# Kernel optimization log

Hardware: AMD Instinct MI355X
Metric: run time of the kernel (lower is better)

## Reference

```python
import jax, jax.numpy as jnp
import numpy as np

N, F, H, C = 50000, 128, 4, 32   # nodes, in_channels, heads, hidden_channels
E, R, DE = 800000, 8, 64         # edges, num_relations, edge_dim


def setup_inputs() -> dict:
    key = jax.random.key(0)
    ks = jax.random.split(key, 10)
    x = jax.random.normal(ks[0], (N, F), dtype=jnp.float32)
    edge_index = jax.random.randint(ks[1], (2, E), 0, N, dtype=jnp.int64)
    edge_type = jax.random.randint(ks[2], (E,), 0, R, dtype=jnp.int64)
    s_in = 1.0 / np.sqrt(F)
    s_e = 1.0 / np.sqrt(DE)
    edge_emb = jax.random.normal(ks[3], (R, DE), dtype=jnp.float32)
    Wq = jax.random.normal(ks[4], (F, H * C), dtype=jnp.float32) * s_in
    Wk = jax.random.normal(ks[5], (F, H * C), dtype=jnp.float32) * s_in
    Wv = jax.random.normal(ks[6], (F, H * C), dtype=jnp.float32) * s_in
    We = jax.random.normal(ks[7], (DE, H * C), dtype=jnp.float32) * s_e
    Wskip = jax.random.normal(ks[8], (F, H * C), dtype=jnp.float32) * s_in
    return {"x": x, "edge_index": edge_index, "edge_type": edge_type,
            "edge_emb": edge_emb, "Wq": Wq, "Wk": Wk, "Wv": Wv,
            "We": We, "Wskip": Wskip}


def reference(x, edge_index, edge_type, edge_emb, Wq, Wk, Wv, We, Wskip):
    # TransformerConv (PyG) with edge embeddings, concat heads, root skip, no bias.
    src, dst = edge_index[0], edge_index[1]
    q = (x @ Wq).reshape(N, H, C)
    k = (x @ Wk).reshape(N, H, C)
    v = (x @ Wv).reshape(N, H, C)
    e = (edge_emb[edge_type] @ We).reshape(E, H, C)      # per-edge relation emb
    kj = k[src] + e                                       # [E,H,C]
    logits = (q[dst] * kj).sum(-1) / jnp.sqrt(jnp.float32(C))  # [E,H]
    # segment softmax over incoming edges of each target node
    m = jax.ops.segment_max(logits, dst, num_segments=N)  # [N,H]
    m = jnp.where(jnp.isfinite(m), m, jnp.float32(0.0))
    ex = jnp.exp(logits - m[dst])
    denom = jax.ops.segment_sum(ex, dst, num_segments=N)  # [N,H]
    alpha = ex / (denom[dst] + 1e-16)                     # [E,H]
    msg = (v[src] + e) * alpha[:, :, None]                # [E,H,C]
    out = jax.ops.segment_sum(msg, dst, num_segments=N).reshape(N, H * C)
    return out + x @ Wskip
```

## Files before the change

kernel.cpp:

```cpp
#include <hip/hip_runtime.h>
#include <hip/hip_bf16.h>

#define NN 50000
#define FF 128
#define NH 4
#define CH 32
#define HC 128
#define NE 800000
#define NR 8
#define DEDIM 64
#define NBLK 196
#define HBLK 3125
#define QBLK 250
#define MTILES 3125

typedef __hip_bfloat16 bf16;
typedef __attribute__((ext_vector_type(8))) short short8;
typedef __attribute__((ext_vector_type(4))) float f32x4;

__device__ __forceinline__ float bflo(unsigned u) { return __uint_as_float(u << 16); }
__device__ __forceinline__ float bfhi(unsigned u) { return __uint_as_float(u & 0xFFFF0000u); }

__device__ __forceinline__ unsigned short f2bf(float f) {
  unsigned u = __float_as_uint(f);
  unsigned r = (u + 0x7FFFu + ((u >> 16) & 1u)) >> 16;
  return (unsigned short)r;
}
__device__ __forceinline__ unsigned pack2bf(float lo, float hi) {
  return (unsigned)f2bf(lo) | ((unsigned)f2bf(hi) << 16);
}

template <int ISBF>
__device__ __forceinline__ float ldf(const void* p, size_t i) {
  if (ISBF) return __bfloat162float(((const bf16*)p)[i]);
  return ((const float*)p)[i];
}

__device__ __forceinline__ int idx_at(const void* p, long long i, int is64) {
  if (is64) { long long v = ((const long long*)p)[i]; return (int)v; }
  return ((const int*)p)[i];
}

__global__ __launch_bounds__(256) void k_prep(const unsigned* __restrict__ xw,
    const int* __restrict__ eidx32, const void* __restrict__ etype,
    const void* __restrict__ emb, const void* __restrict__ We,
    int* __restrict__ flag, int* __restrict__ hist, float* __restrict__ ee,
    unsigned* __restrict__ drk, int* __restrict__ setp) {
  __shared__ float es[NR * DEDIM];
  __shared__ int nzIdx, badBf;
  if (blockIdx.x < HBLK) {
    unsigned long long b = __ballot(eidx32[2 * (threadIdx.x & 63) + 1] != 0);
    int is64 = (b == 0ULL);
    int e = blockIdx.x * 256 + threadIdx.x;
    int src = idx_at(eidx32, e, is64);
    int dst = idx_at(eidx32, (long long)NE + e, is64);
    int et  = idx_at(etype, e, is64);
    src = min(max(src, 0), NN - 1);
    dst = min(max(dst, 0), NN - 1);
    et  = min(max(et, 0), NR - 1);
    int rank = atomicAdd(&hist[dst], 1);
    drk[e]  = ((unsigned)dst << 16) | ((unsigned)rank & 0xFFFFu);
    setp[e] = (src << 3) | et;
    return;
  }
  if (threadIdx.x == 0) { nzIdx = 0; badBf = 0; }
  __syncthreads();
  if (threadIdx.x < 128) {
    if (eidx32[2 * threadIdx.x + 1] != 0) atomicAdd(&nzIdx, 1);
    unsigned e = (xw[threadIdx.x] >> 7) & 0xFFu;
    if (e < 90u || e > 140u) atomicAdd(&badBf, 1);
  }
  __syncthreads();
  const int isbf = (badBf == 0);
  if (threadIdx.x == 0) { flag[0] = (nzIdx == 0); flag[1] = isbf; }
  for (int i = threadIdx.x; i < NR * DEDIM; i += 256)
    es[i] = isbf ? ldf<1>(emb, i) : ldf<0>(emb, i);
  __syncthreads();
  for (int o = threadIdx.x; o < NR * HC; o += 256) {
    int r = o >> 7, j = o & 127;
    float acc = 0.f;
    if (isbf) { for (int d = 0; d < DEDIM; ++d) acc += es[r * DEDIM + d] * ldf<1>(We, d * HC + j); }
    else      { for (int d = 0; d < DEDIM; ++d) acc += es[r * DEDIM + d] * ldf<0>(We, d * HC + j); }
    ee[o] = acc;
  }
}

template <int ISBF>
__device__ __forceinline__ void stage_nat(const void* __restrict__ W,
                                          unsigned short* __restrict__ w) {
  if (ISBF) {
    const uint4* s = (const uint4*)W;
    uint4* d = (uint4*)w;
    for (int i = threadIdx.x; i < FF * HC / 8; i += 256) d[i] = s[i];
  } else {
    const float4* s = (const float4*)W;
    short8* d = (short8*)w;
    for (int i = threadIdx.x; i < FF * HC / 8; i += 256) {
      float4 a = s[2 * i], b = s[2 * i + 1];
      short8 o;
      o[0] = (short)f2bf(a.x); o[1] = (short)f2bf(a.y);
      o[2] = (short)f2bf(a.z); o[3] = (short)f2bf(a.w);
      o[4] = (short)f2bf(b.x); o[5] = (short)f2bf(b.y);
      o[6] = (short)f2bf(b.z); o[7] = (short)f2bf(b.w);
      d[i] = o;
    }
  }
}

__device__ __forceinline__ void hoist_nat(const unsigned short* __restrict__ w,
                                          int wv, int quad, int lr,
                                          short8 bf[2][4]) {
#pragma unroll
  for (int t = 0; t < 2; ++t) {
    int ncol = wv * 32 + t * 16 + lr;
#pragma unroll
    for (int kb = 0; kb < 4; ++kb) {
      short8 v;
#pragma unroll
      for (int j = 0; j < 8; ++j)
        v[j] = (short)w[(kb * 32 + quad * 8 + j) * HC + ncol];
      bf[t][kb] = v;
    }
  }
}

template <int ISBF>
__device__ __forceinline__ void qkvs4_body(const void* __restrict__ x,
    const void* __restrict__ Wq, const void* __restrict__ Ws,
    const void* __restrict__ Wk, const void* __restrict__ Wv,
    unsigned short* __restrict__ qb, unsigned* __restrict__ kvb,
    void* __restrict__ out, unsigned short* __restrict__ wt4,
    unsigned char* __restrict__ est) {
  const int tid  = threadIdx.x;
  const int lane = tid & 63;
  const int wv   = tid >> 6;
  const int quad = lane >> 4;
  const int lr   = lane & 15;
  stage_nat<ISBF>(Wq, wt4 + 0 * FF * HC);
  stage_nat<ISBF>(Ws, wt4 + 1 * FF * HC);
  stage_nat<ISBF>(Wk, wt4 + 2 * FF * HC);
  stage_nat<ISBF>(Wv, wt4 + 3 * FF * HC);
  __syncthreads();
  short8 bf[4][2][4];
#pragma unroll
  for (int m = 0; m < 4; ++m)
    hoist_nat(wt4 + m * FF * HC, wv, quad, lr, bf[m]);
  unsigned short* qs  = (unsigned short*)est;
  unsigned short* sbs = (unsigned short*)(est + 4096);
  float*          sfs = (float*)(est + 4096);
  unsigned*       kvs = (unsigned*)est;
  const unsigned short* xu = (const unsigned short*)x;
  const float* xf = (const float*)x;
  const int mc = blockIdx.x;
  short8 lda[4];
  float4 raw[8];
  {
    size_t off = (size_t)(mc * 16 + lr) * FF + quad * 8;
    if (ISBF) {
#pragma unroll
      for (int kb = 0; kb < 4; ++kb) lda[kb] = *(const short8*)(xu + off + kb * 32);
    } else {
#pragma unroll
      for (int kb = 0; kb < 4; ++kb) {
        raw[2 * kb]     = *(const float4*)(xf + off + kb * 32);
        raw[2 * kb + 1] = *(const float4*)(xf + off + kb * 32 + 4);
      }
    }
  }
  for (int mt = mc; mt < MTILES; mt += QBLK) {
    int m0 = mt * 16;
    short8 cur[4];
    if (ISBF) {
#pragma unroll
      for (int kb = 0; kb < 4; ++kb) cur[kb] = lda[kb];
    } else {
#pragma unroll
      for (int kb = 0; kb < 4; ++kb) {
        float4 a = raw[2 * kb], b = raw[2 * kb + 1];
        short8 o;
        o[0] = (short)f2bf(a.x); o[1] = (short)f2bf(a.y);
        o[2] = (short)f2bf(a.z); o[3] = (short)f2bf(a.w);
        o[4] = (short)f2bf(b.x); o[5] = (short)f2bf(b.y);
        o[6] = (short)f2bf(b.z); o[7] = (short)f2bf(b.w);
        cur[kb] = o;
      }
    }
    int mtn = mt + QBLK;
    if (mtn < MTILES) {
      size_t off = (size_t)(mtn * 16 + lr) * FF + quad * 8;
      if (ISBF) {
#pragma unroll
        for (int kb = 0; kb < 4; ++kb) lda[kb] = *(const short8*)(xu + off + kb * 32);
      } else {
#pragma unroll
        for (int kb = 0; kb < 4; ++kb) {
          raw[2 * kb]     = *(const float4*)(xf + off + kb * 32);
          raw[2 * kb + 1] = *(const float4*)(xf + off + kb * 32 + 4);
        }
      }
    }
    f32x4 acc[4][2];
#pragma unroll
    for (int m = 0; m < 4; ++m)
#pragma unroll
      for (int t = 0; t < 2; ++t) acc[m][t] = {0.f, 0.f, 0.f, 0.f};
#pragma unroll
    for (int kb = 0; kb < 4; ++kb)
#pragma unroll
      for (int m = 0; m < 4; ++m) {
        acc[m][0] = __builtin_amdgcn_mfma_f32_16x16x32_bf16(cur[kb], bf[m][0][kb], acc[m][0], 0, 0, 0);
        acc[m][1] = __builtin_amdgcn_mfma_f32_16x16x32_bf16(cur[kb], bf[m][1][kb], acc[m][1], 0, 0, 0);
      }
#pragma unroll
    for (int t = 0; t < 2; ++t)
#pragma unroll
      for (int r = 0; r < 4; ++r) {
        int li = (quad * 4 + r) * HC + wv * 32 + t * 16 + lr;
        qs[li] = f2bf(acc[0][t][r]);
        if (ISBF) sbs[li] = f2bf(acc[1][t][r]);
        else      sfs[li] = acc[1][t][r];
      }
    __syncthreads();
    {
      int row = tid >> 4, seg = tid & 15;
      *(uint4*)(qb + (size_t)(m0 + row) * HC + seg * 8) = ((const uint4*)qs)[tid];
      if (ISBF) {
        *(uint4*)((unsigned short*)out + (size_t)(m0 + row) * HC + seg * 8) =
            ((const uint4*)sbs)[tid];
      } else {
#pragma unroll
        for (int s = 0; s < 2; ++s) {
          int idx = s * 256 + tid, rw = idx >> 5, sg = idx & 31;
          *(uint4*)((float*)out + (size_t)(m0 + rw) * HC + sg * 4) =
              ((const uint4*)sfs)[idx];
        }
      }
    }
    __syncthreads();
#pragma unroll
    for (int t = 0; t < 2; ++t)
#pragma unroll
      for (int r = 0; r < 4; ++r) {
        int li = (quad * 4 + r) * HC + wv * 32 + t * 16 + lr;
        kvs[li] = pack2bf(acc[2][t][r], acc[3][t][r]);
      }
    __syncthreads();
#pragma unroll
    for (int s = 0; s < 2; ++s) {
      int idx = s * 256 + tid, rw = idx >> 5, sg = idx & 31;
      *(uint4*)(kvb + (size_t)(m0 + rw) * HC + sg * 4) = ((const uint4*)kvs)[idx];
    }
    __syncthreads();
  }
}

__global__ __launch_bounds__(256, 1) void k_qkvs(const unsigned* __restrict__ xw,
    const void* __restrict__ Wq, const void* __restrict__ Ws,
    const void* __restrict__ Wk, const void* __restrict__ Wv,
    unsigned short* __restrict__ qb, unsigned* __restrict__ kvb,
    void* __restrict__ out) {
  __shared__ __align__(16) unsigned short wt4[4 * FF * HC];
  __shared__ __align__(16) unsigned char  est[12288];
  unsigned ex = (xw[threadIdx.x & 63] >> 7) & 0xFFu;
  unsigned long long bb = __ballot(ex < 90u || ex > 140u);
  int isbf = (bb == 0ULL);
  if (isbf) qkvs4_body<1>(xw, Wq, Ws, Wk, Wv, qb, kvb, out, wt4, est);
  else      qkvs4_body<0>(xw, Wq, Ws, Wk, Wv, qb, kvb, out, wt4, est);
}

__global__ __launch_bounds__(256) void k_scan1(const int* __restrict__ hist,
                                               int* __restrict__ bsum) {
  __shared__ int red[4];
  int i = blockIdx.x * 256 + threadIdx.x;
  int v = (i < NN) ? hist[i] : 0;
#pragma unroll
  for (int m = 1; m < 64; m <<= 1) v += __shfl_xor(v, m);
  if ((threadIdx.x & 63) == 0) red[threadIdx.x >> 6] = v;
  __syncthreads();
  if (threadIdx.x == 0) bsum[blockIdx.x] = red[0] + red[1] + red[2] + red[3];
}

__global__ __launch_bounds__(256) void k_scan13(const int* __restrict__ hist,
    const int* __restrict__ bsum, int* __restrict__ rowptr) {
  __shared__ int s[256];
  int t = threadIdx.x;
  int bv = (t < NBLK) ? bsum[t] : 0;
  s[t] = bv;
  __syncthreads();
  for (int off = 1; off < 256; off <<= 1) {
    int u = (t >= off) ? s[t - off] : 0;
    __syncthreads();
    s[t] += u;
    __syncthreads();
  }
  int bexc = (blockIdx.x == 0) ? 0 : s[blockIdx.x - 1];
  __syncthreads();
  int i = blockIdx.x * 256 + t;
  int v = (i < NN) ? hist[i] : 0;
  s[t] = v;
  __syncthreads();
  for (int off = 1; off < 256; off <<= 1) {
    int u = (t >= off) ? s[t - off] : 0;
    __syncthreads();
    s[t] += u;
    __syncthreads();
  }
  int excl = bexc + s[t] - v;
  if (i < NN) rowptr[i] = excl;
  if (i == 0) rowptr[NN] = NE;
}

__global__ __launch_bounds__(256) void k_scatter(const unsigned* __restrict__ drk,
    const int* __restrict__ setp, const int* __restrict__ rowptr,
    int* __restrict__ srcet) {
  int e = blockIdx.x * 256 + threadIdx.x;
  unsigned d = drk[e];
  int pos = rowptr[d >> 16] + (int)(d & 0xFFFFu);
  pos = min(max(pos, 0), NE - 1);
  srcet[pos] = setp[e];
}

__global__ __launch_bounds__(256) void k_gather(const int* __restrict__ rowptr,
    const int* __restrict__ srcet, const unsigned short* __restrict__ qb,
    const unsigned* __restrict__ kvb, const float* __restrict__ ee,
    const int* __restrict__ flag, void* __restrict__ out) {
  int n = blockIdx.x * 4 + (threadIdx.x >> 6);
  int l = threadIdx.x & 63;
  int t = l >> 5;
  int w = l & 31;
  int j0 = ((w >> 3) << 5) + ((w & 7) << 2);
  int beg = __builtin_amdgcn_readfirstlane(rowptr[n]);
  int end = __builtin_amdgcn_readfirstlane(rowptr[n + 1]);
  uint2 qw = *(const uint2*)(qb + (size_t)n * HC + j0);
  float q0 = bflo(qw.x), q1 = bfhi(qw.x), q2 = bflo(qw.y), q3 = bfhi(qw.y);
  const float sc = 0.17677669529663687f;
  float dn = 0.f, a0 = 0.f, a1 = 0.f, a2 = 0.f, a3 = 0.f;
  int p = beg;
  for (; p + 8 <= end; p += 8) {
    int se[4]; uint4 kv[4]; float4 ev[4];
#pragma unroll
    for (int u = 0; u < 4; ++u) se[u] = srcet[p + 2 * u + t];
#pragma unroll
    for (int u = 0; u < 4; ++u)
      kv[u] = *(const uint4*)(kvb + (size_t)(se[u] >> 3) * HC + j0);
#pragma unroll
    for (int u = 0; u < 4; ++u)
      ev[u] = *(const float4*)(ee + ((se[u] & 7) << 7) + j0);
#pragma unroll
    for (int u = 0; u < 4; ++u) {
      float pp = q0 * (bflo(kv[u].x) + ev[u].x) + q1 * (bflo(kv[u].y) + ev[u].y)
               + q2 * (bflo(kv[u].z) + ev[u].z) + q3 * (bflo(kv[u].w) + ev[u].w);
      pp += __shfl_xor(pp, 1);
      pp += __shfl_xor(pp, 2);
      pp += __shfl_xor(pp, 4);
      float xx = __expf(pp * sc);
      dn += xx;
      a0 += (bfhi(kv[u].x) + ev[u].x) * xx;
      a1 += (bfhi(kv[u].y) + ev[u].y) * xx;
      a2 += (bfhi(kv[u].z) + ev[u].z) * xx;
      a3 += (bfhi(kv[u].w) + ev[u].w) * xx;
    }
  }
  if (p < end) {
    int se[4]; bool ok[4]; uint4 kv[4]; float4 ev[4];
#pragma unroll
    for (int u = 0; u < 4; ++u) {
      int pe = p + 2 * u + t;
      ok[u] = pe < end;
      se[u] = srcet[ok[u] ? pe : beg];
    }
#pragma unroll
    for (int u = 0; u < 4; ++u)
      kv[u] = *(const uint4*)(kvb + (size_t)(se[u] >> 3) * HC + j0);
#pragma unroll
    for (int u = 0; u < 4; ++u)
      ev[u] = *(const float4*)(ee + ((se[u] & 7) << 7) + j0);
#pragma unroll
    for (int u = 0; u < 4; ++u) {
      float pp = q0 * (bflo(kv[u].x) + ev[u].x) + q1 * (bflo(kv[u].y) + ev[u].y)
               + q2 * (bflo(kv[u].z) + ev[u].z) + q3 * (bflo(kv[u].w) + ev[u].w);
      pp += __shfl_xor(pp, 1);
      pp += __shfl_xor(pp, 2);
      pp += __shfl_xor(pp, 4);
      float xx = ok[u] ? __expf(pp * sc) : 0.f;
      dn += xx;
      a0 += (bfhi(kv[u].x) + ev[u].x) * xx;
      a1 += (bfhi(kv[u].y) + ev[u].y) * xx;
      a2 += (bfhi(kv[u].z) + ev[u].z) * xx;
      a3 += (bfhi(kv[u].w) + ev[u].w) * xx;
    }
  }
  dn += __shfl_xor(dn, 32);
  a0 += __shfl_xor(a0, 32);
  a1 += __shfl_xor(a1, 32);
  a2 += __shfl_xor(a2, 32);
  a3 += __shfl_xor(a3, 32);
  if (t == 0) {
    float inv = 1.f / (dn + 1e-16f);
    size_t oi = (size_t)n * HC + j0;
    if (flag[1]) {
      uint2 sk = *(const uint2*)((const unsigned short*)out + oi);
      uint2 o;
      o.x = pack2bf(a0 * inv + bflo(sk.x), a1 * inv + bfhi(sk.x));
      o.y = pack2bf(a2 * inv + bflo(sk.y), a3 * inv + bfhi(sk.y));
      *(uint2*)((unsigned short*)out + oi) = o;
    } else {
      float4 sk = *(const float4*)((const float*)out + oi);
      float4 o = make_float4(a0 * inv + sk.x, a1 * inv + sk.y,
                             a2 * inv + sk.z, a3 * inv + sk.w);
      *(float4*)((float*)out + oi) = o;
    }
  }
}

extern "C" void kernel_launch(void* const* d_in, const int* in_sizes, int n_in,
                              void* d_out, int out_size, void* d_ws, size_t ws_size,
                              hipStream_t stream) {
  const void* x     = d_in[0];
  const void* eidx  = d_in[1];
  const void* etype = d_in[2];
  const void* emb   = d_in[3];
  const void* Wq    = d_in[4];
  const void* Wk    = d_in[5];
  const void* Wv    = d_in[6];
  const void* We    = d_in[7];
  const void* Ws    = d_in[8];

  float* base   = (float*)d_ws;
  int*   flag   = (int*)base;
  float* ee     = base + 16;
  int*   rowptr = (int*)(base + 1040);
  int*   bsum   = (int*)(base + 51044);
  int*   srcet  = (int*)(base + 101568);
  int*   hist   = srcet;
  unsigned* drk = (unsigned*)(base + 901568);
  int*   setp   = (int*)(base + 1701568);
  unsigned short* qb  = (unsigned short*)(base + 2501568);
  unsigned*       kvb = (unsigned*)(base + 5701568);

  hipMemsetAsync(hist, 0, NN * sizeof(int), stream);
  k_prep   <<<HBLK + 1, 256, 0, stream>>>((const unsigned*)x, (const int*)eidx,
                                          etype, emb, We, flag, hist, ee,
                                          drk, setp);
  k_qkvs   <<<QBLK, 256, 0, stream>>>((const unsigned*)x, Wq, Ws, Wk, Wv,
                                      qb, kvb, d_out);
  k_scan1  <<<NBLK, 256, 0, stream>>>(hist, bsum);
  k_scan13 <<<NBLK, 256, 0, stream>>>(hist, bsum, rowptr);
  k_scatter<<<HBLK, 256, 0, stream>>>(drk, setp, rowptr, srcet);
  k_gather <<<NN / 4, 256, 0, stream>>>(rowptr, srcet, qb, kvb, ee, flag, d_out);
}
```

Before: 265.1 us.

## Pre-transpose weights in a separate kernel, vectorize edge prep and scatter

Adds a small kernel that converts and transposes the four projection weights into a bf16 buffer in the workspace. The QKV kernel can then load its MFMA B-fragments directly with vector loads instead of staging 128KB in shared memory. Dropping that shared buffer allows two blocks per CU and a grid of 625 blocks. Edge preprocessing and scatter now handle four edges per thread with 128-bit loads and stores, which cuts block count and per-edge load instructions. The cost is an extra launch and more per-thread register pressure.

After: 256.0 us. 1.04x faster.

```diff
diff --git a/kernel.cpp b/kernel.cpp
--- a/kernel.cpp
+++ b/kernel.cpp
@@ -10,8 +10,8 @@
 #define NR 8
 #define DEDIM 64
 #define NBLK 196
-#define HBLK 3125
-#define QBLK 250
+#define PBLK 782
+#define QKB 625
 #define MTILES 3125
 
 typedef __hip_bfloat16 bf16;
@@ -36,9 +36,18 @@
   return ((const float*)p)[i];
 }
 
-__device__ __forceinline__ int idx_at(const void* p, long long i, int is64) {
-  if (is64) { long long v = ((const long long*)p)[i]; return (int)v; }
-  return ((const int*)p)[i];
+__global__ __launch_bounds__(256) void k_wt(const unsigned* __restrict__ xw,
+    const void* __restrict__ Wq, const void* __restrict__ Ws,
+    const void* __restrict__ Wk, const void* __restrict__ Wv,
+    unsigned short* __restrict__ wtr) {
+  unsigned ex = (xw[threadIdx.x & 63] >> 7) & 0xFFu;
+  unsigned long long bb = __ballot(ex < 90u || ex > 140u);
+  int isbf = (bb == 0ULL);
+  int i = blockIdx.x * 256 + threadIdx.x;
+  int m = i >> 14, n = (i >> 7) & 127, k = i & 127;
+  const void* W = (m == 0) ? Wq : (m == 1) ? Ws : (m == 2) ? Wk : Wv;
+  wtr[i] = isbf ? ((const unsigned short*)W)[k * HC + n]
+                : f2bf(((const float*)W)[k * HC + n]);
 }
 
 __global__ __launch_bounds__(256) void k_prep(const unsigned* __restrict__ xw,
@@ -48,19 +57,43 @@
     unsigned* __restrict__ drk, int* __restrict__ setp) {
   __shared__ float es[NR * DEDIM];
   __shared__ int nzIdx, badBf;
-  if (blockIdx.x < HBLK) {
+  if (blockIdx.x < PBLK) {
     unsigned long long b = __ballot(eidx32[2 * (threadIdx.x & 63) + 1] != 0);
     int is64 = (b == 0ULL);
-    int e = blockIdx.x * 256 + threadIdx.x;
-    int src = idx_at(eidx32, e, is64);
-    int dst = idx_at(eidx32, (long long)NE + e, is64);
-    int et  = idx_at(etype, e, is64);
-    src = min(max(src, 0), NN - 1);
-    dst = min(max(dst, 0), NN - 1);
-    et  = min(max(et, 0), NR - 1);
-    int rank = atomicAdd(&hist[dst], 1);
-    drk[e]  = ((unsigned)dst << 16) | ((unsigned)rank & 0xFFFFu);
-    setp[e] = (src << 3) | et;
+    int e0 = (blockIdx.x * 256 + threadIdx.x) * 4;
+    if (e0 >= NE) return;
+    int src[4], dst[4], et[4];
+    if (is64) {
+      const int4* p4 = (const int4*)eidx32;
+      int4 a = p4[e0 >> 1],         b2 = p4[(e0 >> 1) + 1];
+      int4 c = p4[(NE + e0) >> 1],  d  = p4[((NE + e0) >> 1) + 1];
+      const int4* t4 = (const int4*)etype;
+      int4 t0 = t4[e0 >> 1], t1 = t4[(e0 >> 1) + 1];
+      src[0] = a.x; src[1] = a.z; src[2] = b2.x; src[3] = b2.z;
+      dst[0] = c.x; dst[1] = c.z; dst[2] = d.x;  dst[3] = d.z;
+      et[0] = t0.x; et[1] = t0.z; et[2] = t1.x;  et[3] = t1.z;
+    } else {
+      const int4* p4 = (const int4*)eidx32;
+      int4 a = p4[e0 >> 2];
+      int4 c = p4[(NE + e0) >> 2];
+      const int4* t4 = (const int4*)etype;
+      int4 t0 = t4[e0 >> 2];
+      src[0] = a.x; src[1] = a.y; src[2] = a.z; src[3] = a.w;
+      dst[0] = c.x; dst[1] = c.y; dst[2] = c.z; dst[3] = c.w;
+      et[0] = t0.x; et[1] = t0.y; et[2] = t0.z; et[3] = t0.w;
+    }
+    unsigned dr[4]; int sp[4];
+#pragma unroll
+    for (int u = 0; u < 4; ++u) {
+      int s  = min(max(src[u], 0), NN - 1);
+      int dd = min(max(dst[u], 0), NN - 1);
+      int tt = min(max(et[u], 0), NR - 1);
+      int rank = atomicAdd(&hist[dd], 1);
+      dr[u] = ((unsigned)dd << 16) | ((unsigned)rank & 0xFFFFu);
+      sp[u] = (s << 3) | tt;
+    }
+    *(uint4*)&drk[e0]  = make_uint4(dr[0], dr[1], dr[2], dr[3]);
+    *(int4*)&setp[e0]  = make_int4(sp[0], sp[1], sp[2], sp[3]);
     return;
   }
   if (threadIdx.x == 0) { nzIdx = 0; badBf = 0; }
@@ -86,65 +119,25 @@
 }
 
 template <int ISBF>
-__device__ __forceinline__ void stage_nat(const void* __restrict__ W,
-                                          unsigned short* __restrict__ w) {
-  if (ISBF) {
-    const uint4* s = (const uint4*)W;
-    uint4* d = (uint4*)w;
-    for (int i = threadIdx.x; i < FF * HC / 8; i += 256) d[i] = s[i];
-  } else {
-    const float4* s = (const float4*)W;
-    short8* d = (short8*)w;
-    for (int i = threadIdx.x; i < FF * HC / 8; i += 256) {
-      float4 a = s[2 * i], b = s[2 * i + 1];
-      short8 o;
-      o[0] = (short)f2bf(a.x); o[1] = (short)f2bf(a.y);
-      o[2] = (short)f2bf(a.z); o[3] = (short)f2bf(a.w);
-      o[4] = (short)f2bf(b.x); o[5] = (short)f2bf(b.y);
-      o[6] = (short)f2bf(b.z); o[7] = (short)f2bf(b.w);
-      d[i] = o;
-    }
-  }
-}
-
-__device__ __forceinline__ void hoist_nat(const unsigned short* __restrict__ w,
-                                          int wv, int quad, int lr,
-                                          short8 bf[2][4]) {
-#pragma unroll
-  for (int t = 0; t < 2; ++t) {
-    int ncol = wv * 32 + t * 16 + lr;
-#pragma unroll
-    for (int kb = 0; kb < 4; ++kb) {
-      short8 v;
-#pragma unroll
-      for (int j = 0; j < 8; ++j)
-        v[j] = (short)w[(kb * 32 + quad * 8 + j) * HC + ncol];
-      bf[t][kb] = v;
-    }
-  }
-}
-
-template <int ISBF>
 __device__ __forceinline__ void qkvs4_body(const void* __restrict__ x,
-    const void* __restrict__ Wq, const void* __restrict__ Ws,
-    const void* __restrict__ Wk, const void* __restrict__ Wv,
+    const unsigned short* __restrict__ wtr,
     unsigned short* __restrict__ qb, unsigned* __restrict__ kvb,
-    void* __restrict__ out, unsigned short* __restrict__ wt4,
-    unsigned char* __restrict__ est) {
+    void* __restrict__ out, unsigned char* __restrict__ est) {
   const int tid  = threadIdx.x;
   const int lane = tid & 63;
   const int wv   = tid >> 6;
   const int quad = lane >> 4;
   const int lr   = lane & 15;
-  stage_nat<ISBF>(Wq, wt4 + 0 * FF * HC);
-  stage_nat<ISBF>(Ws, wt4 + 1 * FF * HC);
-  stage_nat<ISBF>(Wk, wt4 + 2 * FF * HC);
-  stage_nat<ISBF>(Wv, wt4 + 3 * FF * HC);
-  __syncthreads();
   short8 bf[4][2][4];
 #pragma unroll
   for (int m = 0; m < 4; ++m)
-    hoist_nat(wt4 + m * FF * HC, wv, quad, lr, bf[m]);
+#pragma unroll
+    for (int t = 0; t < 2; ++t) {
+      int ncol = wv * 32 + t * 16 + lr;
+#pragma unroll
+      for (int kb = 0; kb < 4; ++kb)
+        bf[m][t][kb] = *(const short8*)&wtr[(m * HC + ncol) * FF + kb * 32 + quad * 8];
+    }
   unsigned short* qs  = (unsigned short*)est;
   unsigned short* sbs = (unsigned short*)(est + 4096);
   float*          sfs = (float*)(est + 4096);
@@ -167,7 +160,7 @@
       }
     }
   }
-  for (int mt = mc; mt < MTILES; mt += QBLK) {
+  for (int mt = mc; mt < MTILES; mt += QKB) {
     int m0 = mt * 16;
     short8 cur[4];
     if (ISBF) {
@@ -185,7 +178,7 @@
         cur[kb] = o;
       }
     }
-    int mtn = mt + QBLK;
+    int mtn = mt + QKB;
     if (mtn < MTILES) {
       size_t off = (size_t)(mtn * 16 + lr) * FF + quad * 8;
       if (ISBF) {
@@ -254,18 +247,16 @@
   }
 }
 
-__global__ __launch_bounds__(256, 1) void k_qkvs(const unsigned* __restrict__ xw,
-    const void* __restrict__ Wq, const void* __restrict__ Ws,
-    const void* __restrict__ Wk, const void* __restrict__ Wv,
+__global__ __launch_bounds__(256, 2) void k_qkvs(const unsigned* __restrict__ xw,
+    const unsigned short* __restrict__ wtr,
     unsigned short* __restrict__ qb, unsigned* __restrict__ kvb,
     void* __restrict__ out) {
-  __shared__ __align__(16) unsigned short wt4[4 * FF * HC];
-  __shared__ __align__(16) unsigned char  est[12288];
+  __shared__ __align__(16) unsigned char est[12288];
   unsigned ex = (xw[threadIdx.x & 63] >> 7) & 0xFFu;
   unsigned long long bb = __ballot(ex < 90u || ex > 140u);
   int isbf = (bb == 0ULL);
-  if (isbf) qkvs4_body<1>(xw, Wq, Ws, Wk, Wv, qb, kvb, out, wt4, est);
-  else      qkvs4_body<0>(xw, Wq, Ws, Wk, Wv, qb, kvb, out, wt4, est);
+  if (isbf) qkvs4_body<1>(xw, wtr, qb, kvb, out, est);
+  else      qkvs4_body<0>(xw, wtr, qb, kvb, out, est);
 }
 
 __global__ __launch_bounds__(256) void k_scan1(const int* __restrict__ hist,
@@ -313,11 +304,18 @@
 __global__ __launch_bounds__(256) void k_scatter(const unsigned* __restrict__ drk,
     const int* __restrict__ setp, const int* __restrict__ rowptr,
     int* __restrict__ srcet) {
-  int e = blockIdx.x * 256 + threadIdx.x;
-  unsigned d = drk[e];
-  int pos = rowptr[d >> 16] + (int)(d & 0xFFFFu);
-  pos = min(max(pos, 0), NE - 1);
-  srcet[pos] = setp[e];
+  int e0 = (blockIdx.x * 256 + threadIdx.x) * 4;
+  if (e0 >= NE) return;
+  uint4 d4 = *(const uint4*)&drk[e0];
+  int4  s4 = *(const int4*)&setp[e0];
+  unsigned dd[4] = {d4.x, d4.y, d4.z, d4.w};
+  int      sp[4] = {s4.x, s4.y, s4.z, s4.w};
+#pragma unroll
+  for (int u = 0; u < 4; ++u) {
+    int pos = rowptr[dd[u] >> 16] + (int)(dd[u] & 0xFFFFu);
+    pos = min(max(pos, 0), NE - 1);
+    srcet[pos] = sp[u];
+  }
 }
 
 __global__ __launch_bounds__(256) void k_gather(const int* __restrict__ rowptr,
@@ -431,6 +429,7 @@
   float* ee     = base + 16;
   int*   rowptr = (int*)(base + 1040);
   int*   bsum   = (int*)(base + 51044);
+  unsigned short* wtr = (unsigned short*)(base + 51568);
   int*   srcet  = (int*)(base + 101568);
   int*   hist   = srcet;
   unsigned* drk = (unsigned*)(base + 901568);
@@ -439,13 +438,13 @@
   unsigned*       kvb = (unsigned*)(base + 5701568);
 
   hipMemsetAsync(hist, 0, NN * sizeof(int), stream);
-  k_prep   <<<HBLK + 1, 256, 0, stream>>>((const unsigned*)x, (const int*)eidx,
+  k_wt     <<<256, 256, 0, stream>>>((const unsigned*)x, Wq, Ws, Wk, Wv, wtr);
+  k_prep   <<<PBLK + 1, 256, 0, stream>>>((const unsigned*)x, (const int*)eidx,
                                           etype, emb, We, flag, hist, ee,
                                           drk, setp);
-  k_qkvs   <<<QBLK, 256, 0, stream>>>((const unsigned*)x, Wq, Ws, Wk, Wv,
-                                      qb, kvb, d_out);
+  k_qkvs   <<<QKB, 256, 0, stream>>>((const unsigned*)x, wtr, qb, kvb, d_out);
   k_scan1  <<<NBLK, 256, 0, stream>>>(hist, bsum);
   k_scan13 <<<NBLK, 256, 0, stream>>>(hist, bsum, rowptr);
-  k_scatter<<<HBLK, 256, 0, stream>>>(drk, setp, rowptr, srcet);
+  k_scatter<<<PBLK, 256, 0, stream>>>(drk, setp, rowptr, srcet);
   k_gather <<<NN / 4, 256, 0, stream>>>(rowptr, srcet, qb, kvb, ee, flag, d_out);
 }
```
